# Kernel optimization log

Hardware: AMD Instinct MI355X
Metric: run time of the kernel (lower is better)

The kernel has to match this reference:

```python
import jax, jax.numpy as jnp
import numpy as np

D, N, K, NC = 768, 128, 25, 3          # d_model, n_spins, K_mc_eval, n_classes
GAMMA, T_MF, DAMPING = 0.25, 25, 0.7   # mean-field Ising constants from config


def _layernorm(x, g, b):
    m = x.mean(-1, keepdims=True)
    v = ((x - m) ** 2).mean(-1, keepdims=True)
    return (x - m) / jnp.sqrt(v + 1e-5) * g + b


def setup_inputs() -> dict:
    key = jax.random.key(0)
    ks = jax.random.split(key, 16)
    B, S = 256, 128
    return {
        'hidden_states': jax.random.normal(ks[0], (B, S, D), jnp.float32),
        'coalitions': (jax.random.uniform(ks[1], (K, N)) < 0.5).astype(jnp.float32),
        'W_v': jax.random.normal(ks[2], (D, D), jnp.float32) * 0.02,
        'scale': jnp.ones((1,), jnp.float32) * 0.1,
        'local_field': jax.random.normal(ks[3], (N,), jnp.float32) * 0.1,
        'J': jax.random.normal(ks[4], (N, N), jnp.float32) * (0.1 / np.sqrt(N)),
        'Wp': jax.random.normal(ks[5], (D, N), jnp.float32) * 0.02,
        'bp': jnp.zeros((N,), jnp.float32),
        'W1': jax.random.normal(ks[6], (N, 256), jnp.float32) * 0.02,
        'b1': jnp.zeros((256,), jnp.float32),
        'g1': jnp.ones((256,), jnp.float32),
        'be1': jnp.zeros((256,), jnp.float32),
        'W2': jax.random.normal(ks[7], (256, 128), jnp.float32) * 0.02,
        'b2': jnp.zeros((128,), jnp.float32),
        'g2': jnp.ones((128,), jnp.float32),
        'be2': jnp.zeros((128,), jnp.float32),
        'W3': jax.random.normal(ks[8], (128, NC), jnp.float32) * 0.02,
        'b3': jnp.zeros((NC,), jnp.float32),
    }


def reference(hidden_states, coalitions, W_v, scale, local_field, J, Wp, bp,
              W1, b1, g1, be1, W2, b2, g2, be2, W3, b3):
    # --- game theory: all K coalition values in one batched pass ----------
    # coalition_value(f, c) = relu(scale * || sum_n c_n f_n W_v ||).
    # Masking then summing is linear in the mask, so contract mask first.
    feats = hidden_states[:, :N, :]                       # [B, N, D]
    cs = jnp.einsum('kn,bnd->bkd', coalitions, feats)     # [B, K, D]
    proj = jnp.einsum('bkd,de->bke', cs, W_v)             # [B, K, D]
    v = jax.nn.relu(jnp.linalg.norm(proj, axis=-1) * scale[0])  # [B, K]
    # Monte-Carlo Shapley: mean(v | spin i in coalition) - mean(v | not in)
    cnt1 = coalitions.sum(0)                              # [N]
    cnt0 = K - cnt1
    sum_w = v @ coalitions                                # [B, N]
    sum_wo = v.sum(1, keepdims=True) - sum_w
    valid = (cnt1 > 0) & (cnt0 > 0)
    shapley = jnp.where(valid,
                        sum_w / jnp.maximum(cnt1, 1.0) - sum_wo / jnp.maximum(cnt0, 1.0),
                        0.0)                              # [B, N]
    # --- mean-field Ising on projected CLS features -----------------------
    pooled = hidden_states[:, 0, :]                       # [B, D] (CLS)
    m0 = jnp.tanh((pooled @ Wp + bp) * 0.1)               # [B, N]
    Jm = J * (1.0 - jnp.eye(N, dtype=J.dtype))            # zero diagonal

    def step(m, _):
        h = local_field + m @ Jm
        new = jnp.tanh(h / GAMMA)
        return DAMPING * new + (1.0 - DAMPING) * m, None

    m, _ = jax.lax.scan(step, m0, None, length=T_MF)
    h_fin = local_field + m @ Jm
    # log(2*cosh(x)) == logaddexp(x, -x), numerically stable
    free_energy = -GAMMA * jnp.sum(jnp.logaddexp(h_fin / GAMMA, -h_fin / GAMMA),
                                   axis=-1, keepdims=True)   # [B, 1]
    # --- classifier head on expected spins --------------------------------
    x = jax.nn.gelu(_layernorm(m @ W1 + b1, g1, be1), approximate=False)
    x = jax.nn.gelu(_layernorm(x @ W2 + b2, g2, be2), approximate=False)
    logits = x @ W3 + b3                                   # [B, NC]
    return logits, free_energy, shapley
```

## Files before the change

kernel.cpp:

```cpp
#include <hip/hip_runtime.h>
#include <math.h>


typedef _Float16 h8 __attribute__((ext_vector_type(8)));
typedef float f4v __attribute__((ext_vector_type(4)));

constexpr int Bq = 256, Dq = 768, Nq = 128, Kq = 25;
constexpr size_t WVT_OFF  = 0;
constexpr size_t CS_OFF   = 1179648;
constexpr size_t PART_OFF = 11010048;
constexpr size_t M0_OFF   = 11112448;

template <int KS>
__device__ __forceinline__ void ldb24(const float* __restrict__ hb2, float* arr) {
  #pragma unroll
  for (int ct = 0; ct < 3; ++ct) {
    const float* hp = hb2 + (size_t)(KS * 32) * 768 + ct * 16;
    #pragma unroll
    for (int j = 0; j < 8; ++j) arr[ct * 8 + j] = hp[(size_t)j * 768];
  }
}

__device__ __forceinline__ void stepk(const float* arr, const h8& a0, const h8& a1,
                                      f4v acc[2][3]) {
  #pragma unroll
  for (int ct = 0; ct < 3; ++ct) {
    h8 bfv;
    #pragma unroll
    for (int j = 0; j < 8; ++j) bfv[j] = (_Float16)arr[ct * 8 + j];
    acc[0][ct] = __builtin_amdgcn_mfma_f32_16x16x32_f16(a0, bfv, acc[0][ct], 0, 0, 0);
    acc[1][ct] = __builtin_amdgcn_mfma_f32_16x16x32_f16(a1, bfv, acc[1][ct], 0, 0, 0);
  }
}

__global__ __launch_bounds__(256, 2) void k1_front(const float* __restrict__ hst,
                                                   const float* __restrict__ coal,
                                                   const float* __restrict__ Wv,
                                                   const float* __restrict__ Wp,
                                                   const float* __restrict__ bp,
                                                   _Float16* __restrict__ wvt,
                                                   _Float16* __restrict__ csf,
                                                   float* __restrict__ m0g) {
  __shared__ float tile[32 * 33];
  __shared__ float part2[256];
  const int t = threadIdx.x;
  const int b = blockIdx.x & 255;
  const int cc = blockIdx.x >> 8;
  const int l = t & 63, w = t >> 6;
  const int colbase = cc * 192;
  const int kb = (l >> 4) * 8;
  const float* hb = hst + (size_t)b * (128 * 768);

  if (blockIdx.x < 576) {
    const int bx = blockIdx.x % 24, by = blockIdx.x / 24;
    const int r = t >> 3, c4 = (t & 7) * 4;
    const float4 v = *reinterpret_cast<const float4*>(Wv + (size_t)(by * 32 + r) * 768 + bx * 32 + c4);
    tile[r * 33 + c4 + 0] = v.x; tile[r * 33 + c4 + 1] = v.y;
    tile[r * 33 + c4 + 2] = v.z; tile[r * 33 + c4 + 3] = v.w;
    __syncthreads();
    _Float16* dp = wvt + (size_t)(bx * 32 + r) * 768 + by * 32 + c4;
    dp[0] = (_Float16)tile[(c4 + 0) * 33 + r];
    dp[1] = (_Float16)tile[(c4 + 1) * 33 + r];
    dp[2] = (_Float16)tile[(c4 + 2) * 33 + r];
    dp[3] = (_Float16)tile[(c4 + 3) * 33 + r];
  }

  h8 afrag[2][4];
  #pragma unroll
  for (int Mt = 0; Mt < 2; ++Mt) {
    const int row = Mt * 16 + (l & 15);
    #pragma unroll
    for (int ks = 0; ks < 4; ++ks) {
      h8 v;
      if (row < 25) {
        const float4 p0 = *reinterpret_cast<const float4*>(coal + row * 128 + ks * 32 + kb);
        const float4 p1 = *reinterpret_cast<const float4*>(coal + row * 128 + ks * 32 + kb + 4);
        v[0] = (_Float16)p0.x; v[1] = (_Float16)p0.y;
        v[2] = (_Float16)p0.z; v[3] = (_Float16)p0.w;
        v[4] = (_Float16)p1.x; v[5] = (_Float16)p1.y;
        v[6] = (_Float16)p1.z; v[7] = (_Float16)p1.w;
      } else {
        #pragma unroll
        for (int j = 0; j < 8; ++j) v[j] = (_Float16)0.f;
      }
      afrag[Mt][ks] = v;
    }
  }

  f4v acc[2][3];
  #pragma unroll
  for (int Mt = 0; Mt < 2; ++Mt)
    #pragma unroll
    for (int ct = 0; ct < 3; ++ct) acc[Mt][ct] = (f4v){0.f, 0.f, 0.f, 0.f};

  const float* hb2 = hb + (size_t)kb * 768 + colbase + w * 48 + (l & 15);
  float ta[24], tb[24];
  ldb24<0>(hb2, ta);
  ldb24<1>(hb2, tb);
  stepk(ta, afrag[0][0], afrag[1][0], acc);
  ldb24<2>(hb2, ta);
  stepk(tb, afrag[0][1], afrag[1][1], acc);
  ldb24<3>(hb2, tb);
  stepk(ta, afrag[0][2], afrag[1][2], acc);
  stepk(tb, afrag[0][3], afrag[1][3], acc);

  #pragma unroll
  for (int Mt = 0; Mt < 2; ++Mt) {
    const int row0 = Mt * 16 + (l >> 4) * 4;
    #pragma unroll
    for (int ct = 0; ct < 3; ++ct) {
      const int col = colbase + (w * 3 + ct) * 16 + (l & 15);
      #pragma unroll
      for (int r = 0; r < 4; ++r) {
        const int rr = row0 + r;
        if (rr < 25)
          csf[((size_t)b * 25 + rr) * 768 + col] = (_Float16)acc[Mt][ct][r];
      }
    }
  }

  if (cc == 0) {
    const int j = t & 127, sg = t >> 7;
    float s = 0.f;
    for (int d = sg * 384; d < sg * 384 + 384; d += 4) {
      const float4 p4 = *reinterpret_cast<const float4*>(hb + d);
      s += p4.x * Wp[(d + 0) * 128 + j] + p4.y * Wp[(d + 1) * 128 + j]
         + p4.z * Wp[(d + 2) * 128 + j] + p4.w * Wp[(d + 3) * 128 + j];
    }
    part2[t] = s;
    __syncthreads();
    if (t < 128) {
      const float a0 = bp[t] + part2[t] + part2[t + 128];
      m0g[b * 128 + t] = tanhf(a0 * 0.1f);
    }
  }
}

__device__ __forceinline__ float bsum4(float v, float* red) {
  #pragma unroll
  for (int o = 32; o > 0; o >>= 1) v += __shfl_down(v, o, 64);
  __syncthreads();
  if ((threadIdx.x & 63) == 0) red[threadIdx.x >> 6] = v;
  __syncthreads();
  return red[0] + red[1] + red[2] + red[3];
}

__global__ __launch_bounds__(512, 1) void k23(
    const _Float16* __restrict__ csA, const _Float16* __restrict__ wvtB,
    float* __restrict__ part,
    const float* __restrict__ Jg,   const float* __restrict__ lf,
    const float* __restrict__ m0g,
    const float* __restrict__ W1, const float* __restrict__ b1,
    const float* __restrict__ g1, const float* __restrict__ be1,
    const float* __restrict__ W2, const float* __restrict__ b2,
    const float* __restrict__ g2, const float* __restrict__ be2,
    const float* __restrict__ W3, const float* __restrict__ b3,
    float* __restrict__ out) {
  __shared__ __align__(16) char lds[2 * (128 + 192) * 64];
  __shared__ __align__(16) float m_sh[128];
  __shared__ float pmf[256];
  __shared__ __align__(16) float x1[256];
  __shared__ float x2[128];
  __shared__ float red[8];
  const int tid = threadIdx.x;

  if (blockIdx.x < 200) {
    char* ldsA0 = lds;
    char* ldsB0 = lds + 8192;
    char* ldsA1 = lds + 20480;
    char* ldsB1p = lds + 28672;
    const int l = tid & 63, w = tid >> 6;
    const int rg = blockIdx.x >> 2, cc = blockIdx.x & 3;
    const size_t rowbase = (size_t)rg * 128;
    const int colbase = cc * 192;
    const int wm = w & 1, wn = w >> 1;

    const int fch = ((l >> 4) ^ (((l & 15) >> 1) & 3)) * 16;
    const int aoff = (l & 15) * 64 + fch;
    const int boff = (l & 15) * 64 + fch;

    const int srow = tid >> 2, sich = tid & 3;
    const int sch = sich ^ ((srow >> 1) & 3);
    const size_t gA_base = (rowbase + srow) * 768 + sich * 8;
    const size_t gB0_base = (size_t)(colbase + srow) * 768 + sich * 8;
    const size_t gB1_base = (size_t)(colbase + 128 + srow) * 768 + sich * 8;
    const int wA = srow * 64 + sch * 16;
    const int wB0 = srow * 64 + sch * 16;
    const int wB1 = (128 + srow) * 64 + sch * 16;

    f4v acc[4][3];
    #pragma unroll
    for (int mt = 0; mt < 4; ++mt)
      #pragma unroll
      for (int nt = 0; nt < 3; ++nt) acc[mt][nt] = (f4v){0.f, 0.f, 0.f, 0.f};

    uint4 ra0 = *reinterpret_cast<const uint4*>(csA + gA_base);
    uint4 rb00 = *reinterpret_cast<const uint4*>(wvtB + gB0_base);
    uint4 rb10 = {0, 0, 0, 0};
    if (tid < 256) rb10 = *reinterpret_cast<const uint4*>(wvtB + gB1_base);
    uint4 ra1 = *reinterpret_cast<const uint4*>(csA + gA_base + 32);
    uint4 rb01 = *reinterpret_cast<const uint4*>(wvtB + gB0_base + 32);
    uint4 rb11 = {0, 0, 0, 0};
    if (tid < 256) rb11 = *reinterpret_cast<const uint4*>(wvtB + gB1_base + 32);

    for (int s = 0; s < 12; ++s) {
      *reinterpret_cast<uint4*>(ldsA0 + wA) = ra0;
      *reinterpret_cast<uint4*>(ldsB0 + wB0) = rb00;
      if (tid < 256) *reinterpret_cast<uint4*>(ldsB0 + wB1) = rb10;
      *reinterpret_cast<uint4*>(ldsA1 + wA) = ra1;
      *reinterpret_cast<uint4*>(ldsB1p + wB0) = rb01;
      if (tid < 256) *reinterpret_cast<uint4*>(ldsB1p + wB1) = rb11;
      if (s < 11) {
        ra0 = *reinterpret_cast<const uint4*>(csA + gA_base + (2 * s + 2) * 32);
        rb00 = *reinterpret_cast<const uint4*>(wvtB + gB0_base + (2 * s + 2) * 32);
        if (tid < 256) rb10 = *reinterpret_cast<const uint4*>(wvtB + gB1_base + (2 * s + 2) * 32);
        ra1 = *reinterpret_cast<const uint4*>(csA + gA_base + (2 * s + 3) * 32);
        rb01 = *reinterpret_cast<const uint4*>(wvtB + gB0_base + (2 * s + 3) * 32);
        if (tid < 256) rb11 = *reinterpret_cast<const uint4*>(wvtB + gB1_base + (2 * s + 3) * 32);
      }
      __syncthreads();
      {
        h8 af[4];
        #pragma unroll
        for (int mt = 0; mt < 4; ++mt)
          af[mt] = *reinterpret_cast<const h8*>(ldsA0 + (wm * 4 + mt) * 1024 + aoff);
        #pragma unroll
        for (int nt = 0; nt < 3; ++nt) {
          const h8 bf = *reinterpret_cast<const h8*>(ldsB0 + (wn * 3 + nt) * 1024 + boff);
          #pragma unroll
          for (int mt = 0; mt < 4; ++mt)
            acc[mt][nt] = __builtin_amdgcn_mfma_f32_16x16x32_f16(af[mt], bf, acc[mt][nt], 0, 0, 0);
        }
      }
      {
        h8 af[4];
        #pragma unroll
        for (int mt = 0; mt < 4; ++mt)
          af[mt] = *reinterpret_cast<const h8*>(ldsA1 + (wm * 4 + mt) * 1024 + aoff);
        #pragma unroll
        for (int nt = 0; nt < 3; ++nt) {
          const h8 bf = *reinterpret_cast<const h8*>(ldsB1p + (wn * 3 + nt) * 1024 + boff);
          #pragma unroll
          for (int mt = 0; mt < 4; ++mt)
            acc[mt][nt] = __builtin_amdgcn_mfma_f32_16x16x32_f16(af[mt], bf, acc[mt][nt], 0, 0, 0);
        }
      }
      __syncthreads();
    }

    float* redw = reinterpret_cast<float*>(lds);
    #pragma unroll
    for (int mt = 0; mt < 4; ++mt) {
      #pragma unroll
      for (int r = 0; r < 4; ++r) {
        float s2 = acc[mt][0][r] * acc[mt][0][r] + acc[mt][1][r] * acc[mt][1][r]
                 + acc[mt][2][r] * acc[mt][2][r];
        s2 += __shfl_xor(s2, 1); s2 += __shfl_xor(s2, 2);
        s2 += __shfl_xor(s2, 4); s2 += __shfl_xor(s2, 8);
        if ((l & 15) == 0) {
          const int row_local = (wm * 4 + mt) * 16 + (l >> 4) * 4 + r;
          redw[row_local * 4 + wn] = s2;
        }
      }
    }
    __syncthreads();
    if (tid < 128) {
      const float tot = redw[tid * 4 + 0] + redw[tid * 4 + 1]
                      + redw[tid * 4 + 2] + redw[tid * 4 + 3];
      part[(size_t)cc * 6400 + rowbase + tid] = tot;
    }
  } else {
    const int t = tid;
    const int b = blockIdx.x - 200;
    const int tn = t & 127, th = t >> 7;

    float Jreg[64];
    if (t < 256) {
      #pragma unroll
      for (int i = 0; i < 64; ++i)
        Jreg[i] = Jg[(size_t)(th * 64 + i) * 128 + tn];
    }

    float mloc = 0.f, lfv = 0.f, Jdg = 0.f;
    if (t < 128) {
      mloc = m0g[b * 128 + t];
      m_sh[t] = mloc;
      lfv = lf[t];
      Jdg = Jg[t * 128 + t];
    }
    __syncthreads();

    float hs = 0.f;
    for (int it = 0; it <= 25; ++it) {
      if (t < 256) {
        float ps0 = 0.f, ps1 = 0.f, ps2 = 0.f, ps3 = 0.f;
        #pragma unroll
        for (int q = 0; q < 16; ++q) {
          const float4 m4 = *reinterpret_cast<const float4*>(m_sh + th * 64 + q * 4);
          ps0 += Jreg[q * 4 + 0] * m4.x;
          ps1 += Jreg[q * 4 + 1] * m4.y;
          ps2 += Jreg[q * 4 + 2] * m4.z;
          ps3 += Jreg[q * 4 + 3] * m4.w;
        }
        pmf[t] = (ps0 + ps1) + (ps2 + ps3);
      }
      __syncthreads();
      if (it < 25) {
        if (t < 128) {
          const float h = lfv - mloc * Jdg + pmf[t] + pmf[t + 128];
          mloc = 0.7f * tanhf(h * 4.0f) + 0.3f * mloc;
          m_sh[t] = mloc;
        }
        __syncthreads();
      } else {
        if (t < 128) hs = lfv - mloc * Jdg + pmf[t] + pmf[t + 128];
      }
    }

    {
      const float a2 = (t < 128) ? fabsf(hs * 4.0f) : 0.f;
      const float fe = (t < 128) ? (a2 + log1pf(expf(-2.f * a2))) : 0.f;
      const float tot = bsum4(fe, red);
      if (t == 0) out[768 + b] = -0.25f * tot;
    }

    float u = 0.f;
    if (t < 256) {
      u = b1[t];
      #pragma unroll 4
      for (int n = 0; n < 128; n += 4) {
        const float4 m4 = *reinterpret_cast<const float4*>(m_sh + n);
        u += m4.x * W1[(n + 0) * 256 + t] + m4.y * W1[(n + 1) * 256 + t]
           + m4.z * W1[(n + 2) * 256 + t] + m4.w * W1[(n + 3) * 256 + t];
      }
    }
    const float mean1 = bsum4(t < 256 ? u : 0.f, red) * (1.f / 256.f);
    const float xm1 = u - mean1;
    const float var1 = bsum4(t < 256 ? xm1 * xm1 : 0.f, red) * (1.f / 256.f);
    if (t < 256) {
      const float xln1 = xm1 * rsqrtf(var1 + 1e-5f) * g1[t] + be1[t];
      x1[t] = 0.5f * xln1 * (1.f + erff(xln1 * 0.70710678118654752f));
    }
    __syncthreads();

    float u2 = 0.f;
    if (t < 128) {
      u2 = b2[t];
      #pragma unroll 4
      for (int n = 0; n < 256; n += 4) {
        const float4 x4 = *reinterpret_cast<const float4*>(x1 + n);
        u2 += x4.x * W2[(n + 0) * 128 + t] + x4.y * W2[(n + 1) * 128 + t]
            + x4.z * W2[(n + 2) * 128 + t] + x4.w * W2[(n + 3) * 128 + t];
      }
    }
    const float mean2 = bsum4(t < 128 ? u2 : 0.f, red) * (1.f / 128.f);
    const float xm2 = u2 - mean2;
    const float var2 = bsum4(t < 128 ? xm2 * xm2 : 0.f, red) * (1.f / 128.f);
    if (t < 128) {
      const float xln2 = xm2 * rsqrtf(var2 + 1e-5f) * g2[t] + be2[t];
      x2[t] = 0.5f * xln2 * (1.f + erff(xln2 * 0.70710678118654752f));
    }
    __syncthreads();

    if (t < 3) {
      float lg = b3[t];
      #pragma unroll 4
      for (int n = 0; n < 128; ++n) lg += x2[n] * W3[n * 3 + t];
      out[b * 3 + t] = lg;
    }
  }
}

__global__ __launch_bounds__(128, 1) void k3b(const float* __restrict__ part,
                                              const float* __restrict__ coal,
                                              const float* __restrict__ scale,
                                              float* __restrict__ out) {
  __shared__ float vsh[32];
  const int t = threadIdx.x, b = blockIdx.x;
  if (t < 25) {
    const float sq = part[b * 25 + t] + part[6400 + b * 25 + t]
                   + part[12800 + b * 25 + t] + part[19200 + b * 25 + t];
    vsh[t] = fmaxf(sqrtf(sq) * scale[0], 0.f);
  }
  __syncthreads();
  float sw = 0.f, c1 = 0.f, vs = 0.f;
  #pragma unroll
  for (int k = 0; k < 25; ++k) {
    const float c = coal[k * 128 + t];
    const float vk = vsh[k];
    sw += c * vk; vs += vk; c1 += c;
  }
  const float c0 = 25.f - c1;
  float shap = 0.f;
  if (c1 > 0.5f && c0 > 0.5f)
    shap = sw / fmaxf(c1, 1.f) - (vs - sw) / fmaxf(c0, 1.f);
  out[1024 + b * 128 + t] = shap;
}

extern "C" void kernel_launch(void* const* d_in, const int* in_sizes, int n_in,
                              void* d_out, int out_size, void* d_ws, size_t ws_size,
                              hipStream_t stream) {
  const float* hst   = (const float*)d_in[0];
  const float* coal  = (const float*)d_in[1];
  const float* Wv    = (const float*)d_in[2];
  const float* scale = (const float*)d_in[3];
  const float* lf    = (const float*)d_in[4];
  const float* Jg    = (const float*)d_in[5];
  const float* Wp    = (const float*)d_in[6];
  const float* bp    = (const float*)d_in[7];
  const float* W1    = (const float*)d_in[8];
  const float* b1    = (const float*)d_in[9];
  const float* g1    = (const float*)d_in[10];
  const float* be1   = (const float*)d_in[11];
  const float* W2    = (const float*)d_in[12];
  const float* b2    = (const float*)d_in[13];
  const float* g2    = (const float*)d_in[14];
  const float* be2   = (const float*)d_in[15];
  const float* W3    = (const float*)d_in[16];
  const float* b3    = (const float*)d_in[17];
  float* out = (float*)d_out;

  char* ws = (char*)d_ws;
  _Float16* wvt = (_Float16*)(ws + WVT_OFF);
  _Float16* csf = (_Float16*)(ws + CS_OFF);
  float* part   = (float*)(ws + PART_OFF);
  float* m0g    = (float*)(ws + M0_OFF);

  hipLaunchKernelGGL(k1_front, dim3(1024), dim3(256), 0, stream,
                     hst, coal, Wv, Wp, bp, wvt, csf, m0g);
  hipLaunchKernelGGL(k23, dim3(456), dim3(512), 0, stream,
                     csf, wvt, part, Jg, lf, m0g,
                     W1, b1, g1, be1, W2, b2, g2, be2, W3, b3, out);
  hipLaunchKernelGGL(k3b, dim3(256), dim3(128), 0, stream,
                     part, coal, scale, out);
}
```

Before: 68.93 us.

## Split CLS projection across all column blocks and interleave GEMM/Ising blocks

The CLS projection pooled@Wp used to run only in the cc==0 blocks of k1_front, which made those blocks carry extra serial work. It is now split over all four column-chunk blocks, each writing a partial sum, and the Ising blocks of k23 add the partials and apply bias and tanh. k23 also interleaves the GEMM blocks with the mean-field blocks in launch order so the long serial Ising blocks start earlier and overlap with the GEMM. The cost is extra partial-sum traffic to the workspace and a four-way reduction in k23.

```diff
diff --git a/kernel.cpp b/kernel.cpp
--- a/kernel.cpp
+++ b/kernel.cpp
@@ -9,7 +9,7 @@
 constexpr size_t WVT_OFF  = 0;
 constexpr size_t CS_OFF   = 1179648;
 constexpr size_t PART_OFF = 11010048;
-constexpr size_t M0_OFF   = 11112448;
+constexpr size_t M0P_OFF  = 11112448;
 
 template <int KS>
 __device__ __forceinline__ void ldb24(const float* __restrict__ hb2, float* arr) {
@@ -37,10 +37,9 @@
                                                    const float* __restrict__ coal,
                                                    const float* __restrict__ Wv,
                                                    const float* __restrict__ Wp,
-                                                   const float* __restrict__ bp,
                                                    _Float16* __restrict__ wvt,
                                                    _Float16* __restrict__ csf,
-                                                   float* __restrict__ m0g) {
+                                                   float* __restrict__ m0p) {
   __shared__ float tile[32 * 33];
   __shared__ float part2[256];
   const int t = threadIdx.x;
@@ -119,20 +118,19 @@
     }
   }
 
-  if (cc == 0) {
+  {
     const int j = t & 127, sg = t >> 7;
+    const int d0 = cc * 192 + sg * 96;
     float s = 0.f;
-    for (int d = sg * 384; d < sg * 384 + 384; d += 4) {
+    for (int d = d0; d < d0 + 96; d += 4) {
       const float4 p4 = *reinterpret_cast<const float4*>(hb + d);
       s += p4.x * Wp[(d + 0) * 128 + j] + p4.y * Wp[(d + 1) * 128 + j]
          + p4.z * Wp[(d + 2) * 128 + j] + p4.w * Wp[(d + 3) * 128 + j];
     }
     part2[t] = s;
     __syncthreads();
-    if (t < 128) {
-      const float a0 = bp[t] + part2[t] + part2[t + 128];
-      m0g[b * 128 + t] = tanhf(a0 * 0.1f);
-    }
+    if (t < 128)
+      m0p[((size_t)cc * 256 + b) * 128 + t] = part2[t] + part2[t + 128];
   }
 }
 
@@ -149,7 +147,7 @@
     const _Float16* __restrict__ csA, const _Float16* __restrict__ wvtB,
     float* __restrict__ part,
     const float* __restrict__ Jg,   const float* __restrict__ lf,
-    const float* __restrict__ m0g,
+    const float* __restrict__ m0p,  const float* __restrict__ bp,
     const float* __restrict__ W1, const float* __restrict__ b1,
     const float* __restrict__ g1, const float* __restrict__ be1,
     const float* __restrict__ W2, const float* __restrict__ b2,
@@ -164,13 +162,23 @@
   __shared__ float red[8];
   const int tid = threadIdx.x;
 
-  if (blockIdx.x < 200) {
+  bool is_k2;
+  int myid;
+  if (blockIdx.x < 400) {
+    is_k2 = ((blockIdx.x & 1) == 0);
+    myid = blockIdx.x >> 1;
+  } else {
+    is_k2 = false;
+    myid = 200 + (blockIdx.x - 400);
+  }
+
+  if (is_k2) {
     char* ldsA0 = lds;
     char* ldsB0 = lds + 8192;
     char* ldsA1 = lds + 20480;
     char* ldsB1p = lds + 28672;
     const int l = tid & 63, w = tid >> 6;
-    const int rg = blockIdx.x >> 2, cc = blockIdx.x & 3;
+    const int rg = myid >> 2, cc = myid & 3;
     const size_t rowbase = (size_t)rg * 128;
     const int colbase = cc * 192;
     const int wm = w & 1, wn = w >> 1;
@@ -271,7 +279,7 @@
     }
   } else {
     const int t = tid;
-    const int b = blockIdx.x - 200;
+    const int b = myid;
     const int tn = t & 127, th = t >> 7;
 
     float Jreg[64];
@@ -283,7 +291,11 @@
 
     float mloc = 0.f, lfv = 0.f, Jdg = 0.f;
     if (t < 128) {
-      mloc = m0g[b * 128 + t];
+      const float raw = m0p[((size_t)0 * 256 + b) * 128 + t]
+                      + m0p[((size_t)1 * 256 + b) * 128 + t]
+                      + m0p[((size_t)2 * 256 + b) * 128 + t]
+                      + m0p[((size_t)3 * 256 + b) * 128 + t];
+      mloc = tanhf((bp[t] + raw) * 0.1f);
       m_sh[t] = mloc;
       lfv = lf[t];
       Jdg = Jg[t * 128 + t];
@@ -424,12 +436,12 @@
   _Float16* wvt = (_Float16*)(ws + WVT_OFF);
   _Float16* csf = (_Float16*)(ws + CS_OFF);
   float* part   = (float*)(ws + PART_OFF);
-  float* m0g    = (float*)(ws + M0_OFF);
+  float* m0p    = (float*)(ws + M0P_OFF);
 
   hipLaunchKernelGGL(k1_front, dim3(1024), dim3(256), 0, stream,
-                     hst, coal, Wv, Wp, bp, wvt, csf, m0g);
+                     hst, coal, Wv, Wp, wvt, csf, m0p);
   hipLaunchKernelGGL(k23, dim3(456), dim3(512), 0, stream,
-                     csf, wvt, part, Jg, lf, m0g,
+                     csf, wvt, part, Jg, lf, m0p, bp,
                      W1, b1, g1, be1, W2, b2, g2, be2, W3, b3, out);
   hipLaunchKernelGGL(k3b, dim3(256), dim3(128), 0, stream,
                      part, coal, scale, out);
```

After: 75.32 us. 1.09x slower.
